# Optimization experiments

Measured on AMD Instinct MI355X. Metric: run time of the kernel, lower is better.

## Reference

```python
import jax, jax.numpy as jnp
import numpy as np

N_NODES = 100000


def _add_self_loops(edge_index, n):
    loop = jnp.arange(n, dtype=edge_index.dtype)
    src = jnp.concatenate([edge_index[0], loop])
    dst = jnp.concatenate([edge_index[1], loop])
    return src, dst


def _gcn_conv(x, W, b, src, dst, n):
    # h = X W, then symmetric-normalized scatter-add over edges (PyG GCNConv)
    h = x @ W
    ones = jnp.ones(src.shape[0], dtype=h.dtype)
    deg = jax.ops.segment_sum(ones, dst, num_segments=n)  # in-degree incl. self loops
    dinv = jnp.where(deg > 0, jax.lax.rsqrt(deg), 0.0)
    norm = dinv[src] * dinv[dst]                           # [E]
    msg = h[src] * norm[:, None]                           # gather + scale
    out = jax.ops.segment_sum(msg, dst, num_segments=n)    # scatter-add
    return out + b


def setup_inputs() -> dict:
    key = jax.random.key(0)
    k1, k2, k3, k4 = jax.random.split(key, 4)
    F, H, C = 128, 128, 16
    x = jax.random.normal(k1, (N_NODES, F), dtype=jnp.float32)
    edge_index = jax.random.randint(k2, (2, 1600000), 0, N_NODES, dtype=jnp.int64)
    W1 = jax.random.normal(k3, (F, H), dtype=jnp.float32) / np.sqrt(F)
    b1 = jnp.zeros((H,), dtype=jnp.float32)
    W2 = jax.random.normal(k4, (H, C), dtype=jnp.float32) / np.sqrt(H)
    b2 = jnp.zeros((C,), dtype=jnp.float32)
    return {"x": x, "edge_index": edge_index, "W1": W1, "b1": b1, "W2": W2, "b2": b2}


def reference(x, edge_index, W1, b1, W2, b2):
    n = x.shape[0]
    src, dst = _add_self_loops(edge_index, n)
    h = _gcn_conv(x, W1, b1, src, dst, n)
    h = jax.nn.relu(h)
    # dropout(p=0.1) treated as identity (deterministic eval-mode reference)
    logits = _gcn_conv(h, W2, b2, src, dst, n)
    return logits, jax.nn.log_softmax(logits, axis=1)
```

## Files before the change

kernel.cpp:

```cpp
#include <hip/hip_runtime.h>
#include <math.h>


#define ELLW 72
#define EPB 16384
#define BSH 9
#define MAXEB 100
#define MAXBK 200

typedef __attribute__((ext_vector_type(8))) short short8;
typedef __attribute__((ext_vector_type(4))) float f32x4;

__device__ __forceinline__ float bf2f(unsigned short u) {
    return __uint_as_float(((unsigned int)u) << 16);
}
__device__ __forceinline__ unsigned short f2bf(float f) {
    unsigned int u = __float_as_uint(f);
    unsigned int r = (u + 0x7fffu + ((u >> 16) & 1u)) >> 16;
    return (unsigned short)r;
}

__global__ void k_prep(unsigned short* __restrict__ h, float* __restrict__ g,
                       const float* __restrict__ W1, unsigned short* __restrict__ wt,
                       int n) {
    int i = blockIdx.x * blockDim.x + threadIdx.x;
    if (i < 16384) {
        int nc = i >> 7, k = i & 127;
        wt[i] = f2bf(W1[k * 128 + nc]);
    }
    if (i < 128) h[(size_t)n * 128 + i] = 0;
    if (i < 16) g[(size_t)n * 16 + i] = 0.f;
}

__global__ void k_hist(const int* __restrict__ dst, int E,
                       int* __restrict__ hist, int nbuck) {
    __shared__ int lh[MAXBK];
    const int t = threadIdx.x, blk = blockIdx.x;
    for (int i = t; i < nbuck; i += 256) lh[i] = 0;
    __syncthreads();
    const int e0 = blk * EPB;
    const int e1 = min(e0 + EPB, E);
    for (int e = e0 + t; e < e1; e += 256)
        atomicAdd(&lh[dst[e] >> BSH], 1);
    __syncthreads();
    for (int i = t; i < nbuck; i += 256)
        hist[blk * nbuck + i] = lh[i];
}

__global__ void k_scan(int* __restrict__ hist, int* __restrict__ bstart,
                       int* __restrict__ bcount, int neb, int nbuck) {
    __shared__ unsigned short lh[MAXEB * MAXBK];
    __shared__ int sc[256];
    const int t = threadIdx.x;
    const int items = neb * nbuck;
    for (int i = t; i < items; i += 256) lh[i] = (unsigned short)hist[i];
    __syncthreads();
    int total = 0;
    if (t < nbuck)
        for (int blk = 0; blk < neb; ++blk) total += lh[blk * nbuck + t];
    sc[t] = total;
    __syncthreads();
    for (int o = 1; o < 256; o <<= 1) {
        int x = 0;
        if (t >= o) x = sc[t - o];
        __syncthreads();
        if (t >= o) sc[t] += x;
        __syncthreads();
    }
    if (t < nbuck) {
        int run = sc[t] - total;
        bstart[t] = run;
        bcount[t] = total;
        for (int blk = 0; blk < neb; ++blk) {
            int idx = blk * nbuck + t;
            int v = lh[idx];
            hist[idx] = run;
            run += v;
        }
    }
}

__global__ void k_bin(const int* __restrict__ src, const int* __restrict__ dst, int E,
                      const int* __restrict__ hist, int* __restrict__ binned, int nbuck) {
    __shared__ int cnt[MAXBK];
    const int t = threadIdx.x, blk = blockIdx.x;
    for (int i = t; i < nbuck; i += 256) cnt[i] = hist[blk * nbuck + i];
    __syncthreads();
    const int e0 = blk * EPB;
    const int e1 = min(e0 + EPB, E);
    for (int e = e0 + t; e < e1; e += 256) {
        int d = dst[e];
        int b = d >> BSH;
        int pos = atomicAdd(&cnt[b], 1);
        binned[pos] = src[e] | ((d & ((1 << BSH) - 1)) << 17);
    }
}

__global__ void k_ell(const int* __restrict__ binned, const int* __restrict__ bstart,
                      const int* __restrict__ bcount, int* __restrict__ deg,
                      int* __restrict__ col, int n) {
    __shared__ int ldeg[1 << BSH];
    const int t = threadIdx.x, b = blockIdx.x;
    const int node0 = b << BSH;
    for (int i = t; i < (1 << BSH); i += 256) ldeg[i] = 0;
    __syncthreads();
    const int st = bstart[b], cv = bcount[b];
    for (int i = t; i < cv; i += 256) {
        int v = binned[st + i];
        int s = v & 0x1FFFF;
        int dl = v >> 17;
        int q = atomicAdd(&ldeg[dl], 1);
        if (q < ELLW) col[(size_t)(node0 + dl) * ELLW + q] = s;
    }
    __syncthreads();
    for (int i = t; i < (1 << BSH); i += 256) {
        int node = node0 + i;
        if (node < n) {
            int dgv = ldeg[i];
            deg[node] = dgv;
            int dc = dgv > ELLW ? ELLW : dgv;
            int kend = (dc + 7) & ~7;
            for (int q = dc; q < kend; ++q) col[(size_t)node * ELLW + q] = n;
        }
    }
}

__global__ void k_gemm1(const float* __restrict__ x, const unsigned short* __restrict__ wt,
                        const int* __restrict__ deg, unsigned short* __restrict__ h,
                        int n) {
    __shared__ unsigned short xs[64 * 136];
    const int t = threadIdx.x;
    const int row0 = blockIdx.x * 64;
    for (int i = t; i < 2048; i += 256) {
        int r = i >> 5, c4 = (i & 31) << 2;
        int gr = row0 + r;
        float4 v = make_float4(0.f, 0.f, 0.f, 0.f);
        if (gr < n) v = *(const float4*)(x + (size_t)gr * 128 + c4);
        ushort4 u;
        u.x = f2bf(v.x); u.y = f2bf(v.y); u.z = f2bf(v.z); u.w = f2bf(v.w);
        *(ushort4*)(xs + r * 136 + c4) = u;
    }
    __syncthreads();
    const int w = t >> 6;
    const int lane = t & 63;
    const int m = lane & 15, q = lane >> 4;
    f32x4 acc[8];
#pragma unroll
    for (int ns = 0; ns < 8; ++ns) acc[ns] = (f32x4){0.f, 0.f, 0.f, 0.f};
#pragma unroll
    for (int kt = 0; kt < 4; ++kt) {
        short8 a = *(const short8*)(xs + (w * 16 + m) * 136 + kt * 32 + q * 8);
#pragma unroll
        for (int ns = 0; ns < 8; ++ns) {
            short8 b = *(const short8*)((const short*)wt + (ns * 16 + m) * 128 + kt * 32 + q * 8);
            acc[ns] = __builtin_amdgcn_mfma_f32_16x16x32_bf16(a, b, acc[ns], 0, 0, 0);
        }
    }
    unsigned short* xsw = xs + (w * 16) * 136;
    float srow[4];
#pragma unroll
    for (int reg = 0; reg < 4; ++reg) {
        int gr = row0 + w * 16 + q * 4 + reg;
        srow[reg] = (gr < n) ? rsqrtf((float)(deg[gr] + 1)) : 0.f;
    }
#pragma unroll
    for (int ns = 0; ns < 8; ++ns)
#pragma unroll
        for (int reg = 0; reg < 4; ++reg)
            xsw[(q * 4 + reg) * 136 + ns * 16 + m] = f2bf(acc[ns][reg] * srow[reg]);
    __syncthreads();
#pragma unroll
    for (int it = 0; it < 8; ++it) {
        int rl = (lane >> 5) + it * 2;
        int off = (lane & 31) * 4;
        int gr = row0 + w * 16 + rl;
        if (gr < n)
            *(ushort4*)(h + (size_t)gr * 128 + off) = *(const ushort4*)(xsw + rl * 136 + off);
    }
}

__global__ __launch_bounds__(256, 2) void k_gather1f(
        const unsigned short* __restrict__ h, const int* __restrict__ deg,
        const int* __restrict__ col, const float* __restrict__ b1,
        const float* __restrict__ W2, float* __restrict__ g, int n) {
    const int t = threadIdx.x;
    const int lane = t & 15;
    const int d = blockIdx.x * 16 + (t >> 4);
    if (d >= n) return;
    int dg = deg[d];
    if (dg > ELLW) dg = ELLW;
    const float dd = rsqrtf((float)(dg + 1));
    const int kend = (dg + 7) & ~7;
    const int* ecol = col + (size_t)d * ELLW;

    float aA[8], aB[8];
    {
        short8 u = *(const short8*)(h + (size_t)d * 128 + lane * 8);
#pragma unroll
        for (int j = 0; j < 8; ++j) {
            aA[j] = bf2f((unsigned short)u[j]);
            aB[j] = 0.f;
        }
    }
    for (int k = 0; k < kend; k += 8) {
        int4 c0 = *(const int4*)(ecol + k);
        int4 c1 = *(const int4*)(ecol + k + 4);
        short8 u0 = *(const short8*)(h + (size_t)c0.x * 128 + lane * 8);
        short8 u1 = *(const short8*)(h + (size_t)c0.y * 128 + lane * 8);
        short8 u2 = *(const short8*)(h + (size_t)c0.z * 128 + lane * 8);
        short8 u3 = *(const short8*)(h + (size_t)c0.w * 128 + lane * 8);
        short8 u4 = *(const short8*)(h + (size_t)c1.x * 128 + lane * 8);
        short8 u5 = *(const short8*)(h + (size_t)c1.y * 128 + lane * 8);
        short8 u6 = *(const short8*)(h + (size_t)c1.z * 128 + lane * 8);
        short8 u7 = *(const short8*)(h + (size_t)c1.w * 128 + lane * 8);
#pragma unroll
        for (int j = 0; j < 8; ++j) {
            aA[j] += bf2f((unsigned short)u0[j]) + bf2f((unsigned short)u2[j]) +
                     bf2f((unsigned short)u4[j]) + bf2f((unsigned short)u6[j]);
            aB[j] += bf2f((unsigned short)u1[j]) + bf2f((unsigned short)u3[j]) +
                     bf2f((unsigned short)u5[j]) + bf2f((unsigned short)u7[j]);
        }
    }
    float y[8];
    const float* b1p = b1 + lane * 8;
#pragma unroll
    for (int j = 0; j < 8; ++j)
        y[j] = fmaxf(fmaf(aA[j] + aB[j], dd, b1p[j]), 0.f);
    const float4* w2v = (const float4*)(W2 + lane * 8 * 16);
    float4 z0 = make_float4(0.f, 0.f, 0.f, 0.f);
    float4 z1 = z0, z2 = z0, z3 = z0;
#pragma unroll
    for (int j = 0; j < 8; ++j) {
        float4 w0 = w2v[j * 4 + 0], w1 = w2v[j * 4 + 1];
        float4 w2 = w2v[j * 4 + 2], w3 = w2v[j * 4 + 3];
        float yj = y[j];
        z0.x = fmaf(yj, w0.x, z0.x); z0.y = fmaf(yj, w0.y, z0.y);
        z0.z = fmaf(yj, w0.z, z0.z); z0.w = fmaf(yj, w0.w, z0.w);
        z1.x = fmaf(yj, w1.x, z1.x); z1.y = fmaf(yj, w1.y, z1.y);
        z1.z = fmaf(yj, w1.z, z1.z); z1.w = fmaf(yj, w1.w, z1.w);
        z2.x = fmaf(yj, w2.x, z2.x); z2.y = fmaf(yj, w2.y, z2.y);
        z2.z = fmaf(yj, w2.z, z2.z); z2.w = fmaf(yj, w2.w, z2.w);
        z3.x = fmaf(yj, w3.x, z3.x); z3.y = fmaf(yj, w3.y, z3.y);
        z3.z = fmaf(yj, w3.z, z3.z); z3.w = fmaf(yj, w3.w, z3.w);
    }
#pragma unroll
    for (int mm = 1; mm < 16; mm <<= 1) {
        z0.x += __shfl_xor(z0.x, mm); z0.y += __shfl_xor(z0.y, mm);
        z0.z += __shfl_xor(z0.z, mm); z0.w += __shfl_xor(z0.w, mm);
        z1.x += __shfl_xor(z1.x, mm); z1.y += __shfl_xor(z1.y, mm);
        z1.z += __shfl_xor(z1.z, mm); z1.w += __shfl_xor(z1.w, mm);
        z2.x += __shfl_xor(z2.x, mm); z2.y += __shfl_xor(z2.y, mm);
        z2.z += __shfl_xor(z2.z, mm); z2.w += __shfl_xor(z2.w, mm);
        z3.x += __shfl_xor(z3.x, mm); z3.y += __shfl_xor(z3.y, mm);
        z3.z += __shfl_xor(z3.z, mm); z3.w += __shfl_xor(z3.w, mm);
    }
    if (lane < 4) {
        float4 z = (lane == 0) ? z0 : (lane == 1) ? z1 : (lane == 2) ? z2 : z3;
        z.x *= dd; z.y *= dd; z.z *= dd; z.w *= dd;
        *(float4*)(g + (size_t)d * 16 + lane * 4) = z;
    }
}

#define FACC(acc, v) \
    acc.x += v.x; acc.y += v.y; acc.z += v.z; acc.w += v.w

__global__ void k_gather2(const float* __restrict__ g, const int* __restrict__ deg,
                          const int* __restrict__ col, const float* __restrict__ b2,
                          float* __restrict__ out, int n) {
    const int t = threadIdx.x;
    const int d = blockIdx.x * 64 + (t >> 2);
    if (d >= n) return;
    const int l = t & 3;
    int dg = deg[d];
    if (dg > ELLW) dg = ELLW;
    const float dd = rsqrtf((float)(dg + 1));
    const int kend = (dg + 7) & ~7;
    const int* ecol = col + (size_t)d * ELLW;

    float4 aA = *(const float4*)(g + (size_t)d * 16 + l * 4);
    float4 aB = make_float4(0.f, 0.f, 0.f, 0.f);
    float4 aC = aB, aD = aB;
    for (int k = 0; k < kend; k += 8) {
        int4 c0 = *(const int4*)(ecol + k);
        int4 c1 = *(const int4*)(ecol + k + 4);
        float4 h0 = *(const float4*)(g + (size_t)c0.x * 16 + l * 4);
        float4 h1 = *(const float4*)(g + (size_t)c0.y * 16 + l * 4);
        float4 h2 = *(const float4*)(g + (size_t)c0.z * 16 + l * 4);
        float4 h3 = *(const float4*)(g + (size_t)c0.w * 16 + l * 4);
        float4 h4 = *(const float4*)(g + (size_t)c1.x * 16 + l * 4);
        float4 h5 = *(const float4*)(g + (size_t)c1.y * 16 + l * 4);
        float4 h6 = *(const float4*)(g + (size_t)c1.z * 16 + l * 4);
        float4 h7 = *(const float4*)(g + (size_t)c1.w * 16 + l * 4);
        FACC(aA, h0); FACC(aB, h1); FACC(aC, h2); FACC(aD, h3);
        FACC(aA, h4); FACC(aB, h5); FACC(aC, h6); FACC(aD, h7);
    }
    float4 bv = *(const float4*)(b2 + l * 4);
    float4 acc;
    acc.x = fmaf(aA.x + aB.x + aC.x + aD.x, dd, bv.x);
    acc.y = fmaf(aA.y + aB.y + aC.y + aD.y, dd, bv.y);
    acc.z = fmaf(aA.z + aB.z + aC.z + aD.z, dd, bv.z);
    acc.w = fmaf(aA.w + aB.w + aC.w + aD.w, dd, bv.w);
    *(float4*)(out + (size_t)d * 16 + l * 4) = acc;
    float m = fmaxf(fmaxf(acc.x, acc.y), fmaxf(acc.z, acc.w));
    m = fmaxf(m, __shfl_xor(m, 1));
    m = fmaxf(m, __shfl_xor(m, 2));
    float e = expf(acc.x - m) + expf(acc.y - m) + expf(acc.z - m) + expf(acc.w - m);
    e += __shfl_xor(e, 1);
    e += __shfl_xor(e, 2);
    float ls = m + logf(e);
    float4 o;
    o.x = acc.x - ls; o.y = acc.y - ls; o.z = acc.z - ls; o.w = acc.w - ls;
    *(float4*)(out + (size_t)n * 16 + (size_t)d * 16 + l * 4) = o;
}

static inline size_t align256(size_t v) { return (v + 255) & ~(size_t)255; }

extern "C" void kernel_launch(void* const* d_in, const int* in_sizes, int n_in,
                              void* d_out, int out_size, void* d_ws, size_t ws_size,
                              hipStream_t stream) {
    const float* x  = (const float*)d_in[0];
    const int*   ei = (const int*)d_in[1];
    const float* W1 = (const float*)d_in[2];
    const float* b1 = (const float*)d_in[3];
    const float* W2 = (const float*)d_in[4];
    const float* b2 = (const float*)d_in[5];
    float* out = (float*)d_out;

    const int n = in_sizes[0] / 128;
    const int E = in_sizes[1] / 2;
    const int* src = ei;
    const int* dst = ei + E;
    const int NEB = (E + EPB - 1) / EPB;
    const int NBUCK = (n + (1 << BSH) - 1) >> BSH;

    char* base = (char*)d_ws;
    size_t off = 0;
    int* deg = (int*)(base + off); off = align256(off + (size_t)n * 4);
    int* col = (int*)(base + off); off = align256(off + (size_t)n * ELLW * 4);
    unsigned short* wt = (unsigned short*)(base + off); off = align256(off + 128 * 128 * 2);
    unsigned short* h = (unsigned short*)(base + off); off = align256(off + ((size_t)n + 1) * 128 * 2);
    float* g = (float*)(base + off); off = align256(off + ((size_t)n + 1) * 16 * 4);
    int* hist = (int*)(base + off); off = align256(off + (size_t)MAXEB * MAXBK * 4);
    int* bstart = (int*)(base + off); off = align256(off + (size_t)MAXBK * 4);
    int* bcount = (int*)(base + off); off = align256(off + (size_t)MAXBK * 4);
    int* binned = (int*)(base + off); off = align256(off + (size_t)E * 4);

    k_prep<<<64, 256, 0, stream>>>(h, g, W1, wt, n);
    k_hist<<<NEB, 256, 0, stream>>>(dst, E, hist, NBUCK);
    k_scan<<<1, 256, 0, stream>>>(hist, bstart, bcount, NEB, NBUCK);
    k_bin<<<NEB, 256, 0, stream>>>(src, dst, E, hist, binned, NBUCK);
    k_ell<<<NBUCK, 256, 0, stream>>>(binned, bstart, bcount, deg, col, n);

    k_gemm1<<<(n + 63) / 64, 256, 0, stream>>>(x, wt, deg, h, n);
    k_gather1f<<<(n + 15) / 16, 256, 0, stream>>>(h, deg, col, b1, W2, g, n);

    k_gather2<<<(n + 63) / 64, 256, 0, stream>>>(g, deg, col, b2, out, n);
}
```

Before: 370.5 us.

## Fuse prep with histogram and ELL build with GEMM; add nontemporal loads/stores

Merges the weight-prep kernel into the histogram kernel, and the ELL construction kernel into the first GEMM via block-index partitioning. Degree is now counted with global atomics in the histogram pass so the GEMM no longer depends on the ELL kernel, and the two can run in one launch. Streaming loads and stores use nontemporal hints. In exchange, this adds a memset plus 1.6M global atomics on deg, and the fused ELL blocks share LDS and register budget with the GEMM blocks.

```diff
diff --git a/kernel.cpp b/kernel.cpp
--- a/kernel.cpp
+++ b/kernel.cpp
@@ -10,6 +10,7 @@
 
 typedef __attribute__((ext_vector_type(8))) short short8;
 typedef __attribute__((ext_vector_type(4))) float f32x4;
+typedef __attribute__((ext_vector_type(4))) int i32x4;
 
 __device__ __forceinline__ float bf2f(unsigned short u) {
     return __uint_as_float(((unsigned int)u) << 16);
@@ -19,29 +20,36 @@
     unsigned int r = (u + 0x7fffu + ((u >> 16) & 1u)) >> 16;
     return (unsigned short)r;
 }
-
-__global__ void k_prep(unsigned short* __restrict__ h, float* __restrict__ g,
-                       const float* __restrict__ W1, unsigned short* __restrict__ wt,
-                       int n) {
-    int i = blockIdx.x * blockDim.x + threadIdx.x;
-    if (i < 16384) {
-        int nc = i >> 7, k = i & 127;
-        wt[i] = f2bf(W1[k * 128 + nc]);
-    }
-    if (i < 128) h[(size_t)n * 128 + i] = 0;
-    if (i < 16) g[(size_t)n * 16 + i] = 0.f;
-}
-
-__global__ void k_hist(const int* __restrict__ dst, int E,
-                       int* __restrict__ hist, int nbuck) {
+__device__ __forceinline__ i32x4 ld_nt_i4(const int* p) {
+    return __builtin_nontemporal_load((const i32x4*)p);
+}
+
+__global__ void k_prep_hist(unsigned short* __restrict__ h, float* __restrict__ g,
+                            const float* __restrict__ W1, unsigned short* __restrict__ wt,
+                            int n, const int* __restrict__ dst, int E,
+                            int* __restrict__ hist, int nbuck, int* __restrict__ deg) {
     __shared__ int lh[MAXBK];
-    const int t = threadIdx.x, blk = blockIdx.x;
+    const int t = threadIdx.x;
+    if (blockIdx.x < 64) {
+        int i = blockIdx.x * 256 + t;
+        if (i < 16384) {
+            int nc = i >> 7, k = i & 127;
+            wt[i] = f2bf(W1[k * 128 + nc]);
+        }
+        if (i < 128) h[(size_t)n * 128 + i] = 0;
+        if (i < 16) g[(size_t)n * 16 + i] = 0.f;
+        return;
+    }
+    const int blk = blockIdx.x - 64;
     for (int i = t; i < nbuck; i += 256) lh[i] = 0;
     __syncthreads();
     const int e0 = blk * EPB;
     const int e1 = min(e0 + EPB, E);
-    for (int e = e0 + t; e < e1; e += 256)
-        atomicAdd(&lh[dst[e] >> BSH], 1);
+    for (int e = e0 + t; e < e1; e += 256) {
+        int d = dst[e];
+        atomicAdd(&lh[d >> BSH], 1);
+        atomicAdd(&deg[d], 1);
+    }
     __syncthreads();
     for (int i = t; i < nbuck; i += 256)
         hist[blk * nbuck + i] = lh[i];
@@ -96,48 +104,50 @@
     }
 }
 
-__global__ void k_ell(const int* __restrict__ binned, const int* __restrict__ bstart,
-                      const int* __restrict__ bcount, int* __restrict__ deg,
-                      int* __restrict__ col, int n) {
-    __shared__ int ldeg[1 << BSH];
-    const int t = threadIdx.x, b = blockIdx.x;
-    const int node0 = b << BSH;
-    for (int i = t; i < (1 << BSH); i += 256) ldeg[i] = 0;
-    __syncthreads();
-    const int st = bstart[b], cv = bcount[b];
-    for (int i = t; i < cv; i += 256) {
-        int v = binned[st + i];
-        int s = v & 0x1FFFF;
-        int dl = v >> 17;
-        int q = atomicAdd(&ldeg[dl], 1);
-        if (q < ELLW) col[(size_t)(node0 + dl) * ELLW + q] = s;
-    }
-    __syncthreads();
-    for (int i = t; i < (1 << BSH); i += 256) {
-        int node = node0 + i;
-        if (node < n) {
-            int dgv = ldeg[i];
-            deg[node] = dgv;
-            int dc = dgv > ELLW ? ELLW : dgv;
-            int kend = (dc + 7) & ~7;
-            for (int q = dc; q < kend; ++q) col[(size_t)node * ELLW + q] = n;
-        }
-    }
-}
-
-__global__ void k_gemm1(const float* __restrict__ x, const unsigned short* __restrict__ wt,
-                        const int* __restrict__ deg, unsigned short* __restrict__ h,
-                        int n) {
+__global__ __launch_bounds__(256) void k_ell_gemm(
+        const int* __restrict__ binned, const int* __restrict__ bstart,
+        const int* __restrict__ bcount, int* __restrict__ col, int n, int nbuck,
+        const float* __restrict__ x, const unsigned short* __restrict__ wt,
+        const int* __restrict__ deg, unsigned short* __restrict__ h) {
     __shared__ unsigned short xs[64 * 136];
     const int t = threadIdx.x;
-    const int row0 = blockIdx.x * 64;
+    if ((int)blockIdx.x < nbuck) {
+        int* ldeg = (int*)xs;
+        const int b = blockIdx.x;
+        const int node0 = b << BSH;
+        for (int i = t; i < (1 << BSH); i += 256) ldeg[i] = 0;
+        __syncthreads();
+        const int st = bstart[b], cv = bcount[b];
+        for (int i = t; i < cv; i += 256) {
+            int v = binned[st + i];
+            int s = v & 0x1FFFF;
+            int dl = v >> 17;
+            int q = atomicAdd(&ldeg[dl], 1);
+            if (q < ELLW)
+                __builtin_nontemporal_store(s, &col[(size_t)(node0 + dl) * ELLW + q]);
+        }
+        __syncthreads();
+        for (int i = t; i < (1 << BSH); i += 256) {
+            int node = node0 + i;
+            if (node < n) {
+                int dgv = ldeg[i];
+                int dc = dgv > ELLW ? ELLW : dgv;
+                int kend = (dc + 7) & ~7;
+                for (int q = dc; q < kend; ++q)
+                    __builtin_nontemporal_store(n, &col[(size_t)node * ELLW + q]);
+            }
+        }
+        return;
+    }
+    const int row0 = ((int)blockIdx.x - nbuck) * 64;
     for (int i = t; i < 2048; i += 256) {
         int r = i >> 5, c4 = (i & 31) << 2;
         int gr = row0 + r;
-        float4 v = make_float4(0.f, 0.f, 0.f, 0.f);
-        if (gr < n) v = *(const float4*)(x + (size_t)gr * 128 + c4);
+        f32x4 v = (f32x4){0.f, 0.f, 0.f, 0.f};
+        if (gr < n)
+            v = __builtin_nontemporal_load((const f32x4*)(x + (size_t)gr * 128 + c4));
         ushort4 u;
-        u.x = f2bf(v.x); u.y = f2bf(v.y); u.z = f2bf(v.z); u.w = f2bf(v.w);
+        u.x = f2bf(v[0]); u.y = f2bf(v[1]); u.z = f2bf(v[2]); u.w = f2bf(v[3]);
         *(ushort4*)(xs + r * 136 + c4) = u;
     }
     __syncthreads();
@@ -203,16 +213,16 @@
         }
     }
     for (int k = 0; k < kend; k += 8) {
-        int4 c0 = *(const int4*)(ecol + k);
-        int4 c1 = *(const int4*)(ecol + k + 4);
-        short8 u0 = *(const short8*)(h + (size_t)c0.x * 128 + lane * 8);
-        short8 u1 = *(const short8*)(h + (size_t)c0.y * 128 + lane * 8);
-        short8 u2 = *(const short8*)(h + (size_t)c0.z * 128 + lane * 8);
-        short8 u3 = *(const short8*)(h + (size_t)c0.w * 128 + lane * 8);
-        short8 u4 = *(const short8*)(h + (size_t)c1.x * 128 + lane * 8);
-        short8 u5 = *(const short8*)(h + (size_t)c1.y * 128 + lane * 8);
-        short8 u6 = *(const short8*)(h + (size_t)c1.z * 128 + lane * 8);
-        short8 u7 = *(const short8*)(h + (size_t)c1.w * 128 + lane * 8);
+        i32x4 c0 = ld_nt_i4(ecol + k);
+        i32x4 c1 = ld_nt_i4(ecol + k + 4);
+        short8 u0 = *(const short8*)(h + (size_t)c0[0] * 128 + lane * 8);
+        short8 u1 = *(const short8*)(h + (size_t)c0[1] * 128 + lane * 8);
+        short8 u2 = *(const short8*)(h + (size_t)c0[2] * 128 + lane * 8);
+        short8 u3 = *(const short8*)(h + (size_t)c0[3] * 128 + lane * 8);
+        short8 u4 = *(const short8*)(h + (size_t)c1[0] * 128 + lane * 8);
+        short8 u5 = *(const short8*)(h + (size_t)c1[1] * 128 + lane * 8);
+        short8 u6 = *(const short8*)(h + (size_t)c1[2] * 128 + lane * 8);
+        short8 u7 = *(const short8*)(h + (size_t)c1[3] * 128 + lane * 8);
 #pragma unroll
         for (int j = 0; j < 8; ++j) {
             aA[j] += bf2f((unsigned short)u0[j]) + bf2f((unsigned short)u2[j]) +
@@ -256,13 +266,11 @@
     }
     if (lane < 4) {
         float4 z = (lane == 0) ? z0 : (lane == 1) ? z1 : (lane == 2) ? z2 : z3;
-        z.x *= dd; z.y *= dd; z.z *= dd; z.w *= dd;
-        *(float4*)(g + (size_t)d * 16 + lane * 4) = z;
-    }
-}
-
-#define FACC(acc, v) \
-    acc.x += v.x; acc.y += v.y; acc.z += v.z; acc.w += v.w
+        f32x4 zz;
+        zz[0] = z.x * dd; zz[1] = z.y * dd; zz[2] = z.z * dd; zz[3] = z.w * dd;
+        __builtin_nontemporal_store(zz, (f32x4*)(g + (size_t)d * 16 + lane * 4));
+    }
+}
 
 __global__ void k_gather2(const float* __restrict__ g, const int* __restrict__ deg,
                           const int* __restrict__ col, const float* __restrict__ b2,
@@ -276,41 +284,38 @@
     const float dd = rsqrtf((float)(dg + 1));
     const int kend = (dg + 7) & ~7;
     const int* ecol = col + (size_t)d * ELLW;
-
-    float4 aA = *(const float4*)(g + (size_t)d * 16 + l * 4);
-    float4 aB = make_float4(0.f, 0.f, 0.f, 0.f);
-    float4 aC = aB, aD = aB;
+    const float* gl = g + l * 4;
+
+    f32x4 aA = *(const f32x4*)(gl + (size_t)d * 16);
+    f32x4 aB = (f32x4){0.f, 0.f, 0.f, 0.f};
+    f32x4 aC = aB, aD = aB;
     for (int k = 0; k < kend; k += 8) {
-        int4 c0 = *(const int4*)(ecol + k);
-        int4 c1 = *(const int4*)(ecol + k + 4);
-        float4 h0 = *(const float4*)(g + (size_t)c0.x * 16 + l * 4);
-        float4 h1 = *(const float4*)(g + (size_t)c0.y * 16 + l * 4);
-        float4 h2 = *(const float4*)(g + (size_t)c0.z * 16 + l * 4);
-        float4 h3 = *(const float4*)(g + (size_t)c0.w * 16 + l * 4);
-        float4 h4 = *(const float4*)(g + (size_t)c1.x * 16 + l * 4);
-        float4 h5 = *(const float4*)(g + (size_t)c1.y * 16 + l * 4);
-        float4 h6 = *(const float4*)(g + (size_t)c1.z * 16 + l * 4);
-        float4 h7 = *(const float4*)(g + (size_t)c1.w * 16 + l * 4);
-        FACC(aA, h0); FACC(aB, h1); FACC(aC, h2); FACC(aD, h3);
-        FACC(aA, h4); FACC(aB, h5); FACC(aC, h6); FACC(aD, h7);
-    }
-    float4 bv = *(const float4*)(b2 + l * 4);
-    float4 acc;
-    acc.x = fmaf(aA.x + aB.x + aC.x + aD.x, dd, bv.x);
-    acc.y = fmaf(aA.y + aB.y + aC.y + aD.y, dd, bv.y);
-    acc.z = fmaf(aA.z + aB.z + aC.z + aD.z, dd, bv.z);
-    acc.w = fmaf(aA.w + aB.w + aC.w + aD.w, dd, bv.w);
-    *(float4*)(out + (size_t)d * 16 + l * 4) = acc;
-    float m = fmaxf(fmaxf(acc.x, acc.y), fmaxf(acc.z, acc.w));
+        i32x4 c0 = ld_nt_i4(ecol + k);
+        i32x4 c1 = ld_nt_i4(ecol + k + 4);
+        f32x4 h0 = *(const f32x4*)(gl + (size_t)c0[0] * 16);
+        f32x4 h1 = *(const f32x4*)(gl + (size_t)c0[1] * 16);
+        f32x4 h2 = *(const f32x4*)(gl + (size_t)c0[2] * 16);
+        f32x4 h3 = *(const f32x4*)(gl + (size_t)c0[3] * 16);
+        f32x4 h4 = *(const f32x4*)(gl + (size_t)c1[0] * 16);
+        f32x4 h5 = *(const f32x4*)(gl + (size_t)c1[1] * 16);
+        f32x4 h6 = *(const f32x4*)(gl + (size_t)c1[2] * 16);
+        f32x4 h7 = *(const f32x4*)(gl + (size_t)c1[3] * 16);
+        aA += h0; aB += h1; aC += h2; aD += h3;
+        aA += h4; aB += h5; aC += h6; aD += h7;
+    }
+    f32x4 bv = *(const f32x4*)(b2 + l * 4);
+    f32x4 acc = (aA + aB + aC + aD) * dd + bv;
+    __builtin_nontemporal_store(acc, (f32x4*)(out + (size_t)d * 16 + l * 4));
+    float m = fmaxf(fmaxf(acc[0], acc[1]), fmaxf(acc[2], acc[3]));
     m = fmaxf(m, __shfl_xor(m, 1));
     m = fmaxf(m, __shfl_xor(m, 2));
-    float e = expf(acc.x - m) + expf(acc.y - m) + expf(acc.z - m) + expf(acc.w - m);
+    float e = expf(acc[0] - m) + expf(acc[1] - m) + expf(acc[2] - m) + expf(acc[3] - m);
     e += __shfl_xor(e, 1);
     e += __shfl_xor(e, 2);
     float ls = m + logf(e);
-    float4 o;
-    o.x = acc.x - ls; o.y = acc.y - ls; o.z = acc.z - ls; o.w = acc.w - ls;
-    *(float4*)(out + (size_t)n * 16 + (size_t)d * 16 + l * 4) = o;
+    f32x4 o;
+    o[0] = acc[0] - ls; o[1] = acc[1] - ls; o[2] = acc[2] - ls; o[3] = acc[3] - ls;
+    __builtin_nontemporal_store(o, (f32x4*)(out + (size_t)n * 16 + (size_t)d * 16 + l * 4));
 }
 
 static inline size_t align256(size_t v) { return (v + 255) & ~(size_t)255; }
@@ -345,14 +350,14 @@
     int* bcount = (int*)(base + off); off = align256(off + (size_t)MAXBK * 4);
     int* binned = (int*)(base + off); off = align256(off + (size_t)E * 4);
 
-    k_prep<<<64, 256, 0, stream>>>(h, g, W1, wt, n);
-    k_hist<<<NEB, 256, 0, stream>>>(dst, E, hist, NBUCK);
+    hipMemsetAsync(deg, 0, (size_t)n * 4, stream);
+
+    k_prep_hist<<<64 + NEB, 256, 0, stream>>>(h, g, W1, wt, n, dst, E, hist, NBUCK, deg);
     k_scan<<<1, 256, 0, stream>>>(hist, bstart, bcount, NEB, NBUCK);
     k_bin<<<NEB, 256, 0, stream>>>(src, dst, E, hist, binned, NBUCK);
-    k_ell<<<NBUCK, 256, 0, stream>>>(binned, bstart, bcount, deg, col, n);
-
-    k_gemm1<<<(n + 63) / 64, 256, 0, stream>>>(x, wt, deg, h, n);
+    k_ell_gemm<<<NBUCK + (n + 63) / 64, 256, 0, stream>>>(
+        binned, bstart, bcount, col, n, NBUCK, x, wt, deg, h);
+
     k_gather1f<<<(n + 15) / 16, 256, 0, stream>>>(h, deg, col, b1, W2, g, n);
-
     k_gather2<<<(n + 63) / 64, 256, 0, stream>>>(g, deg, col, b2, out, n);
 }
```

After: 453.6 us. +22.4%, slower.
